# Kernel tuning notes

Hardware: AMD Instinct MI355X
Metric: run time of the kernel (lower is better)

## Reference

```python
import jax, jax.numpy as jnp
import numpy as np

V, D, N, DK, DV, H, DFF = 32000, 512, 6, 64, 64, 8, 2048
B, S = 8, 512
EPS = 1e-5


def _pe(seq_len, d_model):
    pos = np.arange(seq_len)[:, None].astype(np.float32)
    i = np.arange(0, d_model, 2).astype(np.float32)
    ang = pos / np.power(10000.0, i / d_model)
    pe = np.zeros((seq_len, d_model), dtype=np.float32)
    pe[:, 0::2] = np.sin(ang)
    pe[:, 1::2] = np.cos(ang)
    return jnp.asarray(pe)


def _ln(x, g, b):
    m = jnp.mean(x, axis=-1, keepdims=True)
    v = jnp.mean(jnp.square(x - m), axis=-1, keepdims=True)
    return (x - m) * jax.lax.rsqrt(v + EPS) * g + b


def _mha(xq, xkv, Wq, Wk, Wv, bq, bk, bv, mask):
    # Wq/Wk: [H,D,DK], Wv: [H,D,DV]; mask: [B,Sq,Skv] additive
    q = jnp.einsum('bsd,hdk->bhsk', xq, Wq) + bq[None, :, None, :]
    k = jnp.einsum('bsd,hdk->bhsk', xkv, Wk) + bk[None, :, None, :]
    v = jnp.einsum('bsd,hdk->bhsk', xkv, Wv) + bv[None, :, None, :]
    scores = jnp.einsum('bhqk,bhsk->bhqs', q, k) / jnp.sqrt(jnp.float32(DK))
    scores = scores + mask[:, None, :, :]
    attn = jax.nn.softmax(scores, axis=-1)
    out = jnp.einsum('bhqs,bhsv->bhqv', attn, v)  # [B,H,Sq,DV]
    return out.transpose(0, 2, 1, 3).reshape(xq.shape[0], xq.shape[1], H * DV)


def setup_inputs() -> dict:
    key = jax.random.key(0)
    ks = jax.random.split(key, 24)
    sc = 0.02
    inp = {
        'decoder_input': jax.random.randint(ks[0], (B, S), 0, V),
        'encoder_output': jax.random.normal(ks[1], (B, S, D), dtype=jnp.float32),
        'self_mask': jnp.where(jnp.tril(jnp.ones((S, S), dtype=bool)), 0.0, -1e9)[None].repeat(B, 0).astype(jnp.float32),
        'cross_mask': jnp.zeros((B, S, S), dtype=jnp.float32),
        'emb': jax.random.normal(ks[2], (V, D), dtype=jnp.float32),
        'Wq_s': jax.random.normal(ks[3], (N, H, D, DK)) * sc,
        'Wk_s': jax.random.normal(ks[4], (N, H, D, DK)) * sc,
        'Wv_s': jax.random.normal(ks[5], (N, H, D, DV)) * sc,
        'bq_s': jnp.zeros((N, H, DK)), 'bk_s': jnp.zeros((N, H, DK)), 'bv_s': jnp.zeros((N, H, DV)),
        'Wq_c': jax.random.normal(ks[6], (N, H, D, DK)) * sc,
        'Wk_c': jax.random.normal(ks[7], (N, H, D, DK)) * sc,
        'Wv_c': jax.random.normal(ks[8], (N, H, D, DV)) * sc,
        'bq_c': jnp.zeros((N, H, DK)), 'bk_c': jnp.zeros((N, H, DK)), 'bv_c': jnp.zeros((N, H, DV)),
        'W1': jax.random.normal(ks[9], (N, D, DFF)) * sc,
        'b1': jnp.zeros((N, DFF)),
        'W2': jax.random.normal(ks[10], (N, DFF, D)) * sc,
        'b2': jnp.zeros((N, D)),
        'ln1_g': jnp.ones((N, D)), 'ln1_b': jnp.zeros((N, D)),
        'ln2_g': jnp.ones((N, D)), 'ln2_b': jnp.zeros((N, D)),
    }
    return inp


def reference(decoder_input, encoder_output, self_mask, cross_mask, emb,
              Wq_s, Wk_s, Wv_s, bq_s, bk_s, bv_s,
              Wq_c, Wk_c, Wv_c, bq_c, bk_c, bv_c,
              W1, b1, W2, b2, ln1_g, ln1_b, ln2_g, ln2_b):
    x = emb[decoder_input] + _pe(decoder_input.shape[1], D)[None]
    for l in range(N):
        sa = _mha(x, x, Wq_s[l], Wk_s[l], Wv_s[l], bq_s[l], bk_s[l], bv_s[l], self_mask)
        x = _ln(x + sa, ln1_g[l], ln1_b[l])
        ca = _mha(x, encoder_output, Wq_c[l], Wk_c[l], Wv_c[l], bq_c[l], bk_c[l], bv_c[l], cross_mask)
        x = _ln(x + ca, ln2_g[l], ln2_b[l])
        ff = jax.nn.relu(jnp.einsum('bsd,df->bsf', x, W1[l]) + b1[l])
        ff = jnp.einsum('bsf,fd->bsd', ff, W2[l]) + b2[l]
        # source reuses layer_norm2 for the third norm (layer_norm3 is dead)
        x = _ln(x + ff, ln2_g[l], ln2_b[l])
    return x
```

## Files before the change

kernel.cpp:

```cpp
#include <hip/hip_runtime.h>
#include <hip/hip_bf16.h>
#include <math.h>

#define BB 8
#define SS 512
#define DDIM 512
#define HH 8
#define DFFV 2048
#define NLAYER 6
#define EPSV 1e-5f
#define WQS 0.180336880f

typedef __attribute__((ext_vector_type(8))) short bf16x8;
typedef __attribute__((ext_vector_type(4))) float f32x4;

static __device__ __forceinline__ ushort f2bf(float f) {
  union { float f; unsigned u; } uf; uf.f = f;
  unsigned u = uf.u;
  unsigned r = (u + 0x7fffu + ((u >> 16) & 1u)) >> 16;
  return (ushort)r;
}
static __device__ __forceinline__ float bf2f(ushort h) {
  union { unsigned u; float f; } x;
  x.u = ((unsigned)h) << 16;
  return x.f;
}

static __device__ __forceinline__ void gload_lds16(const void* g, void* l) {
  __builtin_amdgcn_global_load_lds(
      (const __attribute__((address_space(1))) void*)g,
      (__attribute__((address_space(3))) void*)l, 16, 0, 0);
}

__global__ __launch_bounds__(256) void embed_pe_kernel(
    const int* __restrict__ idx, const float* __restrict__ emb,
    ushort* __restrict__ xb) {
  int t = blockIdx.x * blockDim.x + threadIdx.x;
  if (t >= BB * SS * DDIM) return;
  int d = t & (DDIM - 1);
  int bs = t >> 9;
  int s = bs & (SS - 1);
  int tok = idx[bs];
  int i2 = d & ~1;
  float ang = (float)s * powf(10000.0f, -((float)i2) / (float)DDIM);
  float pe = (d & 1) ? cosf(ang) : sinf(ang);
  float v = emb[tok * DDIM + d] + pe;
  xb[t] = f2bf(v);
}

__global__ __launch_bounds__(256) void cast_bf16_kernel(
    const float* __restrict__ in, ushort* __restrict__ out, int n4) {
  int t = blockIdx.x * blockDim.x + threadIdx.x;
  if (t >= n4) return;
  float4 v = reinterpret_cast<const float4*>(in)[t];
  ushort4 o;
  o.x = f2bf(v.x); o.y = f2bf(v.y); o.z = f2bf(v.z); o.w = f2bf(v.w);
  reinterpret_cast<ushort4*>(out)[t] = o;
}

__global__ __launch_bounds__(256) void wtrans_kernel(
    const float* __restrict__ in, ushort* __restrict__ out, int R, int C,
    int lgH, size_t zl, float scale) {
  __shared__ float t[32][33];
  int z = blockIdx.z;
  int l = z >> lgH, hh = z & ((1 << lgH) - 1);
  const float* ip = in + (size_t)z * R * C;
  ushort* op = out + (size_t)l * zl + (size_t)hh * R * C;
  int j = threadIdx.x & 31, i0 = threadIdx.x >> 5;
  int r0 = blockIdx.y * 32, c0 = blockIdx.x * 32;
#pragma unroll
  for (int p = 0; p < 4; p++) {
    int r = r0 + i0 + p * 8;
    t[i0 + p * 8][j] = ip[(size_t)r * C + c0 + j];
  }
  __syncthreads();
#pragma unroll
  for (int p = 0; p < 4; p++) {
    int cc = c0 + i0 + p * 8;
    op[(size_t)cc * R + r0 + j] = f2bf(t[j][i0 + p * 8] * scale);
  }
}

__global__ __launch_bounds__(256) void pack_bias_kernel(
    const float* __restrict__ bq, const float* __restrict__ bk,
    const float* __restrict__ bv, const float* __restrict__ bkc,
    const float* __restrict__ bvc, const float* __restrict__ bqc,
    float* __restrict__ qkvb, float* __restrict__ ckvb,
    float* __restrict__ cqb) {
  int t = blockIdx.x * 256 + threadIdx.x;
  if (t < NLAYER * 1536) {
    int l = t / 1536, n = t % 1536;
    float v = n < 512 ? bq[l * 512 + n] * WQS
                      : (n < 1024 ? bk[l * 512 + n - 512] : bv[l * 512 + n - 1024]);
    qkvb[t] = v;
  }
  if (t < NLAYER * 1024) {
    int l = t / 1024, n = t % 1024;
    ckvb[t] = n < 512 ? bkc[l * 512 + n] : bvc[l * 512 + n - 512];
  }
  if (t < NLAYER * 512) cqb[t] = bqc[t] * WQS;
}

template <int BM, int BN, int RELU, int OUTBF, int NTV, int LGP, int SPLITK,
          int SWZ>
__global__ __launch_bounds__(256) void gemm_mfma(
    const ushort* __restrict__ A, const ushort* __restrict__ Bw,
    const float* __restrict__ bias, float* __restrict__ Cf,
    ushort* __restrict__ Cb, ushort* __restrict__ vt, int M, int N, int K) {
  constexpr int WM = BM / 64;
  constexpr int WN = 4 / WM;
  constexpr int W = BN / WN;
  constexpr int AF = 4;
  constexpr int BF = W / 16;
  constexpr int GA = BM * 8;
  constexpr int GPT = (BM + BN) * 8 / 256;
  __shared__ __align__(16) ushort lds_s[2][(BM + BN) * 64];
  int bn, bm;
  if (SWZ) {
    int nwg = gridDim.x * gridDim.y;
    int wg = blockIdx.y * gridDim.x + blockIdx.x;
    int cpx = nwg >> 3;
    int swz = (wg & 7) * cpx + (wg >> 3);
    bn = (swz % gridDim.x) * BN;
    bm = (swz / gridDim.x) * BM;
  } else {
    bn = blockIdx.x * BN;
    bm = blockIdx.y * BM;
  }
  int kz = (SPLITK > 1) ? blockIdx.z : 0;
  int Keff = K / SPLITK;
  int kbase = kz * Keff;
  int tid = threadIdx.x, lane = tid & 63, w = tid >> 6;
  int wm = w / WN, wn = w % WN;
  int c = lane & 15, g16 = lane >> 4;
  f32x4 acc[AF][BF] = {};

  auto STAGE = [&](int k0, int bufi) {
#pragma unroll
    for (int i = 0; i < GPT; i++) {
      int gidx = i * 256 + tid;
      int gbase = (i * 4 + w) * 64;
      const ushort* src;
      if (gidx < GA) {
        int row = gidx >> 3, dg = gidx & 7;
        src = A + (size_t)(bm + row) * K + kbase + k0 + ((dg ^ (row & 7)) << 3);
      } else {
        int bidx = gidx - GA;
        int row = bidx >> 3, dg = bidx & 7;
        src = Bw + (size_t)(bn + row) * K + kbase + k0 + ((dg ^ (row & 7)) << 3);
      }
      gload_lds16(src, (void*)((char*)(&lds_s[bufi][0]) + gbase * 16));
    }
  };

  int nk = Keff >> 6;
  STAGE(0, 0);
  for (int kt = 0; kt < nk; kt++) {
    int cur = kt & 1;
    if (kt + 1 < nk) {
      STAGE((kt + 1) << 6, cur ^ 1);
      asm volatile("s_waitcnt vmcnt(%0)" ::"n"(GPT) : "memory");
    } else {
      asm volatile("s_waitcnt vmcnt(0)" ::: "memory");
    }
    __builtin_amdgcn_s_barrier();
    __builtin_amdgcn_sched_barrier(0);
    const ushort* Alds = &lds_s[cur][0];
    const ushort* Blds = &lds_s[cur][BM * 64];
#pragma unroll
    for (int ks = 0; ks < 2; ks++) {
      int g = ks * 4 + g16;
      bf16x8 a[AF], b[BF];
#pragma unroll
      for (int i = 0; i < AF; i++) {
        int R = wm * 64 + i * 16 + c;
        a[i] = *(const bf16x8*)(Alds + R * 64 + ((g ^ (R & 7)) << 3));
      }
#pragma unroll
      for (int j = 0; j < BF; j++) {
        int Rb = wn * W + j * 16 + c;
        b[j] = *(const bf16x8*)(Blds + Rb * 64 + ((g ^ (Rb & 7)) << 3));
      }
#pragma unroll
      for (int i = 0; i < AF; i++)
#pragma unroll
        for (int j = 0; j < BF; j++)
          acc[i][j] = __builtin_amdgcn_mfma_f32_16x16x32_bf16(a[i], b[j],
                                                              acc[i][j], 0, 0, 0);
    }
    __builtin_amdgcn_sched_barrier(0);
    __builtin_amdgcn_s_barrier();
  }
  int rb = g16 * 4;
#pragma unroll
  for (int j = 0; j < BF; j++) {
    int col = bn + wn * W + j * 16 + c;
    float bv = (SPLITK > 1 && kz != 0) ? 0.0f : bias[col];
    int cc = LGP ? (col & ((1 << LGP) - 1)) : col;
    int lp = LGP ? (col >> LGP) : 0;
    if (NTV > 0 && cc >= NTV) {
      int hh = (cc - NTV) >> 6, dv = col & 63;
      ushort* vtl = vt + (size_t)lp * 2097152;
#pragma unroll
      for (int i = 0; i < AF; i++) {
        int row = bm + wm * 64 + i * 16 + rb;
        int b_ = row >> 9, s_ = row & 511;
        ushort4 o4;
        o4.x = f2bf(acc[i][j][0] + bv);
        o4.y = f2bf(acc[i][j][1] + bv);
        o4.z = f2bf(acc[i][j][2] + bv);
        o4.w = f2bf(acc[i][j][3] + bv);
        *reinterpret_cast<ushort4*>(
            vtl + ((size_t)(b_ * 8 + hh) * 64 + dv) * 512 + s_) = o4;
      }
    } else {
#pragma unroll
      for (int i = 0; i < AF; i++) {
#pragma unroll
        for (int qq = 0; qq < 4; qq++) {
          int row = bm + wm * 64 + i * 16 + rb + qq;
          float v = acc[i][j][qq] + bv;
          if (RELU) v = fmaxf(v, 0.0f);
          if (OUTBF)
            Cb[(size_t)row * N + col] = f2bf(v);
          else
            Cf[(size_t)kz * M * N + (size_t)row * N + col] = v;
        }
      }
    }
  }
}

template <int MASKED, int NW>
__global__ __launch_bounds__(NW * 64) void attn_mfma(
    const ushort* __restrict__ q, int qstr, const ushort* __restrict__ k,
    int kstr, const ushort* __restrict__ vt, ushort* __restrict__ out) {
  __shared__ __align__(16) char lds[32768 + NW * 2048];
  int q0 = blockIdx.x * (NW * 16), h = blockIdx.y, b = blockIdx.z;
  int tid = threadIdx.x, lane = tid & 63, w = tid >> 6;
  int c = lane & 15, g16 = lane >> 4, rb = g16 * 4;

  bf16x8 qa[2];
#pragma unroll
  for (int ks = 0; ks < 2; ks++)
    qa[ks] = *(const bf16x8*)(q + (size_t)(b * SS + q0 + 16 * w + c) * qstr +
                              h * 64 + ks * 32 + g16 * 8);
  f32x4 o[4] = {};
  float mq = -1e30f, lq = 0.f;

  int nt = MASKED ? (q0 >> 6) + 1 : 8;
  int pbase = 32768 + w * 2048;

  constexpr int GPTK = 512 / (NW * 64);
  bf16x8 rk[GPTK], rv[GPTK];
  const ushort* vbase = vt + ((size_t)(b * 8 + h) * 64) * 512;
  auto LOADT = [&](int kv0) {
#pragma unroll
    for (int i = 0; i < GPTK; i++) {
      int idx = tid + i * (NW * 64);
      int row = idx >> 3, gw = idx & 7;
      rk[i] = *(const bf16x8*)(k + (size_t)(b * SS + kv0 + row) * kstr +
                               h * 64 + gw * 8);
      rv[i] = *(const bf16x8*)(vbase + (size_t)row * 512 + kv0 + gw * 8);
    }
  };
  auto WRT = [&](int bufi) {
    char* p = lds + bufi * 16384;
#pragma unroll
    for (int i = 0; i < GPTK; i++) {
      int idx = tid + i * (NW * 64);
      int row = idx >> 3, gw = idx & 7;
      *(bf16x8*)(p + row * 128 + ((gw ^ (row & 7)) << 4)) = rk[i];
      *(bf16x8*)(p + 8192 + row * 128 + ((gw ^ (row & 7)) << 4)) = rv[i];
    }
  };
  LOADT(0);
  WRT(0);
  for (int t = 0; t < nt; t++) {
    if (t + 1 < nt) LOADT((t + 1) * 64);
    __syncthreads();
    char* kb_ = lds + (t & 1) * 16384;
    char* vb_ = kb_ + 8192;
    f32x4 sp[4] = {};
    __builtin_amdgcn_s_setprio(1);
#pragma unroll
    for (int ks = 0; ks < 2; ks++) {
      int g = ks * 4 + g16;
#pragma unroll
      for (int f = 0; f < 4; f++) {
        int row = f * 16 + c;
        bf16x8 k8 = *(bf16x8*)(kb_ + row * 128 + ((g ^ (row & 7)) << 4));
        sp[f] = __builtin_amdgcn_mfma_f32_16x16x32_bf16(k8, qa[ks], sp[f], 0, 0, 0);
      }
    }
    __builtin_amdgcn_s_setprio(0);
    if (MASKED && t == nt - 1) {
      int ql = 16 * w + c;
#pragma unroll
      for (int f = 0; f < 4; f++)
#pragma unroll
        for (int j = 0; j < 4; j++)
          sp[f][j] += (f * 16 + rb + j) <= ql ? 0.0f : -1e9f;
    }
    float tmax = -1e30f;
#pragma unroll
    for (int f = 0; f < 4; f++)
#pragma unroll
      for (int j = 0; j < 4; j++) tmax = fmaxf(tmax, sp[f][j]);
    tmax = fmaxf(tmax, __shfl_xor(tmax, 16));
    tmax = fmaxf(tmax, __shfl_xor(tmax, 32));
    float mn = fmaxf(mq, tmax);
    float scq = exp2f(mq - mn);
    float psum = 0.f;
#pragma unroll
    for (int f = 0; f < 4; f++)
#pragma unroll
      for (int j = 0; j < 4; j++) {
        float pv = exp2f(sp[f][j] - mn);
        sp[f][j] = pv;
        psum += pv;
      }
    psum += __shfl_xor(psum, 16);
    psum += __shfl_xor(psum, 32);
    lq = lq * scq + psum;
    mq = mn;
    int sb = lane & 48;
#pragma unroll
    for (int j = 0; j < 4; j++) {
      float scj = __shfl(scq, sb | (rb + j));
      o[0][j] *= scj; o[1][j] *= scj; o[2][j] *= scj; o[3][j] *= scj;
    }
#pragma unroll
    for (int f = 0; f < 4; f++) {
      int kv0 = f * 16 + rb;
      ushort4 pk;
      pk.x = f2bf(sp[f][0]); pk.y = f2bf(sp[f][1]);
      pk.z = f2bf(sp[f][2]); pk.w = f2bf(sp[f][3]);
      int gg = kv0 >> 3, off = (kv0 & 7) * 2;
      *(ushort4*)(lds + pbase + c * 128 + (((gg) ^ (c & 7)) << 4) + off) = pk;
    }
    __builtin_amdgcn_s_setprio(1);
#pragma unroll
    for (int ks2 = 0; ks2 < 2; ks2++) {
      int g = ks2 * 4 + g16;
      bf16x8 pa = *(bf16x8*)(lds + pbase + c * 128 + ((g ^ (c & 7)) << 4));
#pragma unroll
      for (int f = 0; f < 4; f++) {
        int row = f * 16 + c;
        bf16x8 v8 = *(bf16x8*)(vb_ + row * 128 + ((g ^ (row & 7)) << 4));
        o[f] = __builtin_amdgcn_mfma_f32_16x16x32_bf16(pa, v8, o[f], 0, 0, 0);
      }
    }
    __builtin_amdgcn_s_setprio(0);
    if (t + 1 < nt) WRT((t + 1) & 1);
  }
  float invq = 1.0f / lq;
  int sb = lane & 48;
#pragma unroll
  for (int j = 0; j < 4; j++) {
    float invj = __shfl(invq, sb | (rb + j));
    size_t rowo = (size_t)(b * SS + q0 + 16 * w + rb + j) * 512 + h * 64;
#pragma unroll
    for (int f = 0; f < 4; f++)
      out[rowo + f * 16 + c] = f2bf(o[f][j] * invj);
  }
}

template <int Y2>
__global__ __launch_bounds__(256) void add_ln_kernel(
    ushort* __restrict__ xb, const ushort* __restrict__ yb,
    const float* __restrict__ y0, const float* __restrict__ y1,
    const float* __restrict__ g, const float* __restrict__ bta,
    float* __restrict__ xf) {
  int row = blockIdx.x * 4 + (threadIdx.x >> 6);
  int lane = threadIdx.x & 63;
  int base = row * DDIM + lane * 8;
  bf16x8 xv = *reinterpret_cast<const bf16x8*>(xb + base);
  float v[8];
  if (Y2) {
    float4 a0 = *reinterpret_cast<const float4*>(y0 + base);
    float4 a1 = *reinterpret_cast<const float4*>(y0 + base + 4);
    float4 c0 = *reinterpret_cast<const float4*>(y1 + base);
    float4 c1 = *reinterpret_cast<const float4*>(y1 + base + 4);
    v[0] = bf2f((ushort)xv[0]) + a0.x + c0.x;
    v[1] = bf2f((ushort)xv[1]) + a0.y + c0.y;
    v[2] = bf2f((ushort)xv[2]) + a0.z + c0.z;
    v[3] = bf2f((ushort)xv[3]) + a0.w + c0.w;
    v[4] = bf2f((ushort)xv[4]) + a1.x + c1.x;
    v[5] = bf2f((ushort)xv[5]) + a1.y + c1.y;
    v[6] = bf2f((ushort)xv[6]) + a1.z + c1.z;
    v[7] = bf2f((ushort)xv[7]) + a1.w + c1.w;
  } else {
    bf16x8 yv = *reinterpret_cast<const bf16x8*>(yb + base);
#pragma unroll
    for (int i = 0; i < 8; i++)
      v[i] = bf2f((ushort)xv[i]) + bf2f((ushort)yv[i]);
  }
  float s = 0.f;
#pragma unroll
  for (int i = 0; i < 8; i++) s += v[i];
#pragma unroll
  for (int off = 32; off > 0; off >>= 1) s += __shfl_xor(s, off);
  float mean = s * (1.0f / DDIM);
  float t2 = 0.f;
#pragma unroll
  for (int i = 0; i < 8; i++) {
    v[i] -= mean;
    t2 += v[i] * v[i];
  }
#pragma unroll
  for (int off = 32; off > 0; off >>= 1) t2 += __shfl_xor(t2, off);
  float rs = rsqrtf(t2 * (1.0f / DDIM) + EPSV);
  int cidx = lane * 8;
  float4 g0 = *reinterpret_cast<const float4*>(g + cidx);
  float4 g1 = *reinterpret_cast<const float4*>(g + cidx + 4);
  float4 b0 = *reinterpret_cast<const float4*>(bta + cidx);
  float4 b1 = *reinterpret_cast<const float4*>(bta + cidx + 4);
  float o[8];
  o[0] = v[0] * rs * g0.x + b0.x; o[1] = v[1] * rs * g0.y + b0.y;
  o[2] = v[2] * rs * g0.z + b0.z; o[3] = v[3] * rs * g0.w + b0.w;
  o[4] = v[4] * rs * g1.x + b1.x; o[5] = v[5] * rs * g1.y + b1.y;
  o[6] = v[6] * rs * g1.z + b1.z; o[7] = v[7] * rs * g1.w + b1.w;
  bf16x8 ob;
#pragma unroll
  for (int i = 0; i < 8; i++) ob[i] = (short)f2bf(o[i]);
  *reinterpret_cast<bf16x8*>(xb + base) = ob;
  if (xf) {
    float4 w0 = {o[0], o[1], o[2], o[3]}, w1 = {o[4], o[5], o[6], o[7]};
    *reinterpret_cast<float4*>(xf + base) = w0;
    *reinterpret_cast<float4*>(xf + base + 4) = w1;
  }
}

extern "C" void kernel_launch(void* const* d_in, const int* in_sizes, int n_in,
                              void* d_out, int out_size, void* d_ws,
                              size_t ws_size, hipStream_t stream) {
  const int* dec = (const int*)d_in[0];
  const float* enc = (const float*)d_in[1];
  const float* emb = (const float*)d_in[4];
  const float* Wq_s = (const float*)d_in[5];
  const float* Wk_s = (const float*)d_in[6];
  const float* Wv_s = (const float*)d_in[7];
  const float* bq_s = (const float*)d_in[8];
  const float* bk_s = (const float*)d_in[9];
  const float* bv_s = (const float*)d_in[10];
  const float* Wq_c = (const float*)d_in[11];
  const float* Wk_c = (const float*)d_in[12];
  const float* Wv_c = (const float*)d_in[13];
  const float* bq_c = (const float*)d_in[14];
  const float* bk_c = (const float*)d_in[15];
  const float* bv_c = (const float*)d_in[16];
  const float* W1 = (const float*)d_in[17];
  const float* b1 = (const float*)d_in[18];
  const float* W2 = (const float*)d_in[19];
  const float* b2 = (const float*)d_in[20];
  const float* ln1_g = (const float*)d_in[21];
  const float* ln1_b = (const float*)d_in[22];
  const float* ln2_g = (const float*)d_in[23];
  const float* ln2_b = (const float*)d_in[24];

  char* ws = (char*)d_ws;
  ushort* wqkv = (ushort*)(ws + 0);
  ushort* wqc = (ushort*)(ws + 9437184ull);
  ushort* wckv = (ushort*)(ws + 12582912ull);
  ushort* w1t = (ushort*)(ws + 18874368ull);
  ushort* w2t = (ushort*)(ws + 31457280ull);
  ushort* encb = (ushort*)(ws + 44040192ull);
  ushort* xb = (ushort*)(ws + 48234496ull);
  ushort* tmpb = (ushort*)(ws + 52428800ull);
  float* tmpf = (float*)(ws + 56623104ull);
  ushort* qkvbuf = (ushort*)(ws + 73400320ull);
  ushort* cq = (ushort*)(ws + 73400320ull);
  ushort* ff1b = (ushort*)(ws + 73400320ull);
  ushort* vt = (ushort*)(ws + 85983232ull);
  float* qkvbias = (float*)(ws + 90177536ull);
  float* ckvbias = (float*)(ws + 90214400ull);
  ushort* ckvbuf = (ushort*)(ws + 90238976ull);
  ushort* vtc = (ushort*)(ws + 140570624ull);
  float* cqbias = (float*)(ws + 165736448ull);

  const int M = BB * SS;
  dim3 g256(256);

  embed_pe_kernel<<<dim3((M * DDIM + 255) / 256), g256, 0, stream>>>(dec, emb,
                                                                     xb);
  cast_bf16_kernel<<<dim3(M * DDIM / 4 / 256), g256, 0, stream>>>(
      enc, encb, M * DDIM / 4);
  pack_bias_kernel<<<dim3(36), g256, 0, stream>>>(bq_s, bk_s, bv_s, bk_c, bv_c,
                                                  bq_c, qkvbias, ckvbias,
                                                  cqbias);

  wtrans_kernel<<<dim3(2, 16, 48), g256, 0, stream>>>(Wq_s, wqkv, 512, 64, 3,
                                                      786432ull, WQS);
  wtrans_kernel<<<dim3(2, 16, 48), g256, 0, stream>>>(Wk_s, wqkv + 262144, 512,
                                                      64, 3, 786432ull, 1.0f);
  wtrans_kernel<<<dim3(2, 16, 48), g256, 0, stream>>>(Wv_s, wqkv + 524288, 512,
                                                      64, 3, 786432ull, 1.0f);
  wtrans_kernel<<<dim3(2, 16, 48), g256, 0, stream>>>(Wq_c, wqc, 512, 64, 3,
                                                      262144ull, WQS);
  wtrans_kernel<<<dim3(2, 16, 48), g256, 0, stream>>>(Wk_c, wckv, 512, 64, 3,
                                                      524288ull, 1.0f);
  wtrans_kernel<<<dim3(2, 16, 48), g256, 0, stream>>>(Wv_c, wckv + 262144, 512,
                                                      64, 3, 524288ull, 1.0f);
  wtrans_kernel<<<dim3(64, 16, 6), g256, 0, stream>>>(W1, w1t, 512, 2048, 0,
                                                      1048576ull, 1.0f);
  wtrans_kernel<<<dim3(16, 64, 6), g256, 0, stream>>>(W2, w2t, 2048, 512, 0,
                                                      1048576ull, 1.0f);

  gemm_mfma<128, 128, 0, 1, 512, 10, 1, 0><<<dim3(48, 32), g256, 0, stream>>>(
      encb, wckv, ckvbias, nullptr, ckvbuf, vtc, M, 6144, 512);

  for (int l = 0; l < NLAYER; l++) {
    gemm_mfma<64, 128, 0, 1, 1024, 0, 1, 1><<<dim3(12, 64), g256, 0, stream>>>(
        xb, wqkv + (size_t)l * 786432, qkvbias + l * 1536, nullptr, qkvbuf, vt,
        M, 1536, 512);
    attn_mfma<1, 4><<<dim3(8, 8, 8), g256, 0, stream>>>(
        qkvbuf, 1536, qkvbuf + 512, 1536, vt, tmpb);
    add_ln_kernel<0><<<dim3(M / 4), g256, 0, stream>>>(
        xb, tmpb, nullptr, nullptr, ln1_g + l * 512, ln1_b + l * 512, nullptr);
    gemm_mfma<64, 64, 0, 1, 0, 0, 1, 1><<<dim3(8, 64), g256, 0, stream>>>(
        xb, wqc + (size_t)l * 262144, cqbias + l * 512, nullptr, cq, nullptr,
        M, 512, 512);
    attn_mfma<0, 8><<<dim3(4, 8, 8), dim3(512), 0, stream>>>(
        cq, 512, ckvbuf + l * 1024, 6144, vtc + (size_t)l * 2097152, tmpb);
    add_ln_kernel<0><<<dim3(M / 4), g256, 0, stream>>>(
        xb, tmpb, nullptr, nullptr, ln2_g + l * 512, ln2_b + l * 512, nullptr);
    gemm_mfma<64, 128, 1, 1, 0, 0, 1, 1><<<dim3(16, 64), g256, 0, stream>>>(
        xb, w1t + (size_t)l * 1048576, b1 + l * DFFV, nullptr, ff1b, nullptr,
        M, DFFV, 512);
    gemm_mfma<64, 128, 0, 0, 0, 0, 2, 1><<<dim3(4, 64, 2), g256, 0, stream>>>(
        ff1b, w2t + (size_t)l * 1048576, b2 + l * 512, tmpf, nullptr, nullptr,
        M, 512, DFFV);
    add_ln_kernel<1><<<dim3(M / 4), g256, 0, stream>>>(
        xb, nullptr, tmpf, tmpf + (size_t)M * 512, ln2_g + l * 512,
        ln2_b + l * 512, (l == NLAYER - 1) ? (float*)d_out : nullptr);
  }
}
```

Baseline: 643.4 us.

## Widen attention KV tiles to 128 and add lazy softmax rescaling

The attention kernel now processes 128 keys per iteration instead of 64. This doubles the LDS buffers for K, V and P, halves the number of tile iterations and barriers, and changes the causal tile count and mask offset to match. It also skips the running-max rescale of the output accumulators when the new tile max exceeds the old max by no more than a threshold across the wave, which saves exp and shuffle work at some cost in numerical headroom. Separately, the cross-attention Q projection GEMM switches to a 64x128 tile. The larger LDS footprint and extra registers may lower occupancy, and the wider causal tile does more masked work on diagonal blocks.

```diff
diff --git a/kernel.cpp b/kernel.cpp
--- a/kernel.cpp
+++ b/kernel.cpp
@@ -235,7 +235,7 @@
 __global__ __launch_bounds__(NW * 64) void attn_mfma(
     const ushort* __restrict__ q, int qstr, const ushort* __restrict__ k,
     int kstr, const ushort* __restrict__ vt, ushort* __restrict__ out) {
-  __shared__ __align__(16) char lds[32768 + NW * 2048];
+  __shared__ __align__(16) char lds[65536 + NW * 4096];
   int q0 = blockIdx.x * (NW * 16), h = blockIdx.y, b = blockIdx.z;
   int tid = threadIdx.x, lane = tid & 63, w = tid >> 6;
   int c = lane & 15, g16 = lane >> 4, rb = g16 * 4;
@@ -248,46 +248,48 @@
   f32x4 o[4] = {};
   float mq = -1e30f, lq = 0.f;
 
-  int nt = MASKED ? (q0 >> 6) + 1 : 8;
-  int pbase = 32768 + w * 2048;
-
-  constexpr int GPTK = 512 / (NW * 64);
+  int nt = MASKED ? (q0 >> 7) + 1 : 4;
+  int pbase = 65536 + w * 4096;
+
+  constexpr int GPTK = 1024 / (NW * 64);
   bf16x8 rk[GPTK], rv[GPTK];
   const ushort* vbase = vt + ((size_t)(b * 8 + h) * 64) * 512;
   auto LOADT = [&](int kv0) {
 #pragma unroll
     for (int i = 0; i < GPTK; i++) {
       int idx = tid + i * (NW * 64);
-      int row = idx >> 3, gw = idx & 7;
-      rk[i] = *(const bf16x8*)(k + (size_t)(b * SS + kv0 + row) * kstr +
-                               h * 64 + gw * 8);
-      rv[i] = *(const bf16x8*)(vbase + (size_t)row * 512 + kv0 + gw * 8);
+      int krow = idx >> 3, kg = idx & 7;
+      rk[i] = *(const bf16x8*)(k + (size_t)(b * SS + kv0 + krow) * kstr +
+                               h * 64 + kg * 8);
+      int dv = idx >> 4, vg = idx & 15;
+      rv[i] = *(const bf16x8*)(vbase + (size_t)dv * 512 + kv0 + vg * 8);
     }
   };
   auto WRT = [&](int bufi) {
-    char* p = lds + bufi * 16384;
+    char* p = lds + bufi * 32768;
 #pragma unroll
     for (int i = 0; i < GPTK; i++) {
       int idx = tid + i * (NW * 64);
-      int row = idx >> 3, gw = idx & 7;
-      *(bf16x8*)(p + row * 128 + ((gw ^ (row & 7)) << 4)) = rk[i];
-      *(bf16x8*)(p + 8192 + row * 128 + ((gw ^ (row & 7)) << 4)) = rv[i];
+      int krow = idx >> 3, kg = idx & 7;
+      *(bf16x8*)(p + krow * 128 + ((kg ^ (krow & 7)) << 4)) = rk[i];
+      int dv = idx >> 4, vg = idx & 15;
+      *(bf16x8*)(p + 16384 + dv * 256 + ((vg ^ (dv & 7)) << 4)) = rv[i];
     }
   };
   LOADT(0);
   WRT(0);
   for (int t = 0; t < nt; t++) {
-    if (t + 1 < nt) LOADT((t + 1) * 64);
+    if (t + 1 < nt) LOADT((t + 1) * 128);
     __syncthreads();
-    char* kb_ = lds + (t & 1) * 16384;
-    char* vb_ = kb_ + 8192;
-    f32x4 sp[4] = {};
+    char* kb_ = lds + (t & 1) * 32768;
+    char* vb_ = kb_ + 16384;
+    f32x4 sp[8] = {};
     __builtin_amdgcn_s_setprio(1);
 #pragma unroll
     for (int ks = 0; ks < 2; ks++) {
       int g = ks * 4 + g16;
 #pragma unroll
-      for (int f = 0; f < 4; f++) {
+      for (int f = 0; f < 8; f++) {
         int row = f * 16 + c;
         bf16x8 k8 = *(bf16x8*)(kb_ + row * 128 + ((g ^ (row & 7)) << 4));
         sp[f] = __builtin_amdgcn_mfma_f32_16x16x32_bf16(k8, qa[ks], sp[f], 0, 0, 0);
@@ -295,59 +297,62 @@
     }
     __builtin_amdgcn_s_setprio(0);
     if (MASKED && t == nt - 1) {
-      int ql = 16 * w + c;
-#pragma unroll
-      for (int f = 0; f < 4; f++)
+      int qrel = q0 + 16 * w + c - t * 128;
+#pragma unroll
+      for (int f = 0; f < 8; f++)
 #pragma unroll
         for (int j = 0; j < 4; j++)
-          sp[f][j] += (f * 16 + rb + j) <= ql ? 0.0f : -1e9f;
+          sp[f][j] += (f * 16 + rb + j) <= qrel ? 0.0f : -1e9f;
     }
     float tmax = -1e30f;
 #pragma unroll
-    for (int f = 0; f < 4; f++)
+    for (int f = 0; f < 8; f++)
 #pragma unroll
       for (int j = 0; j < 4; j++) tmax = fmaxf(tmax, sp[f][j]);
     tmax = fmaxf(tmax, __shfl_xor(tmax, 16));
     tmax = fmaxf(tmax, __shfl_xor(tmax, 32));
-    float mn = fmaxf(mq, tmax);
-    float scq = exp2f(mq - mn);
+    if (!__all(tmax <= mq + 4.0f)) {
+      float mn = fmaxf(mq, tmax);
+      float scq = exp2f(mq - mn);
+      mq = mn;
+      lq *= scq;
+      int sb = lane & 48;
+#pragma unroll
+      for (int j = 0; j < 4; j++) {
+        float scj = __shfl(scq, sb | (rb + j));
+        o[0][j] *= scj; o[1][j] *= scj; o[2][j] *= scj; o[3][j] *= scj;
+      }
+    }
     float psum = 0.f;
 #pragma unroll
-    for (int f = 0; f < 4; f++)
+    for (int f = 0; f < 8; f++)
 #pragma unroll
       for (int j = 0; j < 4; j++) {
-        float pv = exp2f(sp[f][j] - mn);
+        float pv = exp2f(sp[f][j] - mq);
         sp[f][j] = pv;
         psum += pv;
       }
     psum += __shfl_xor(psum, 16);
     psum += __shfl_xor(psum, 32);
-    lq = lq * scq + psum;
-    mq = mn;
-    int sb = lane & 48;
-#pragma unroll
-    for (int j = 0; j < 4; j++) {
-      float scj = __shfl(scq, sb | (rb + j));
-      o[0][j] *= scj; o[1][j] *= scj; o[2][j] *= scj; o[3][j] *= scj;
-    }
-#pragma unroll
-    for (int f = 0; f < 4; f++) {
-      int kv0 = f * 16 + rb;
+    lq += psum;
+#pragma unroll
+    for (int f = 0; f < 8; f++) {
+      int kv0l = f * 16 + rb;
       ushort4 pk;
       pk.x = f2bf(sp[f][0]); pk.y = f2bf(sp[f][1]);
       pk.z = f2bf(sp[f][2]); pk.w = f2bf(sp[f][3]);
-      int gg = kv0 >> 3, off = (kv0 & 7) * 2;
-      *(ushort4*)(lds + pbase + c * 128 + (((gg) ^ (c & 7)) << 4) + off) = pk;
+      int gg = kv0l >> 3, off = (kv0l & 7) * 2;
+      *(ushort4*)(lds + pbase + c * 256 + ((gg ^ (c & 7)) << 4) + off) = pk;
     }
     __builtin_amdgcn_s_setprio(1);
 #pragma unroll
-    for (int ks2 = 0; ks2 < 2; ks2++) {
+    for (int ks2 = 0; ks2 < 4; ks2++) {
       int g = ks2 * 4 + g16;
-      bf16x8 pa = *(bf16x8*)(lds + pbase + c * 128 + ((g ^ (c & 7)) << 4));
+      bf16x8 pa = *(bf16x8*)(lds + pbase + c * 256 + ((g ^ (c & 7)) << 4));
 #pragma unroll
       for (int f = 0; f < 4; f++) {
         int row = f * 16 + c;
-        bf16x8 v8 = *(bf16x8*)(vb_ + row * 128 + ((g ^ (row & 7)) << 4));
+        bf16x8 v8 = *(bf16x8*)(vb_ + row * 256 + ((g ^ (row & 7)) << 4));
         o[f] = __builtin_amdgcn_mfma_f32_16x16x32_bf16(pa, v8, o[f], 0, 0, 0);
       }
     }
@@ -518,7 +523,7 @@
         qkvbuf, 1536, qkvbuf + 512, 1536, vt, tmpb);
     add_ln_kernel<0><<<dim3(M / 4), g256, 0, stream>>>(
         xb, tmpb, nullptr, nullptr, ln1_g + l * 512, ln1_b + l * 512, nullptr);
-    gemm_mfma<64, 64, 0, 1, 0, 0, 1, 1><<<dim3(8, 64), g256, 0, stream>>>(
+    gemm_mfma<64, 128, 0, 1, 0, 0, 1, 1><<<dim3(4, 64), g256, 0, stream>>>(
         xb, wqc + (size_t)l * 262144, cqbias + l * 512, nullptr, cq, nullptr,
         M, 512, 512);
     attn_mfma<0, 8><<<dim3(4, 8, 8), dim3(512), 0, stream>>>(
```

Result: no change. 647.0 us (+0.6%).
